# Optimization experiments

Hardware: AMD Instinct MI355X
Metric: run time of the kernel (lower is better)

## Reference

```python
import jax, jax.numpy as jnp
import numpy as np

B, N, F_IN, F_OUT, K = 128, 400, 128, 128, 5


def setup_inputs() -> dict:
    key = jax.random.key(0)
    ks = jax.random.split(key, 7)
    s_in = 1.0 / np.sqrt(F_IN)
    s_out = 1.0 / np.sqrt(F_OUT)
    return {
        "x": jax.random.normal(ks[0], (B, N, F_IN), dtype=jnp.float32),
        # SAGEConv layer 1: lin_l (neighbor agg, with bias) and lin_r (root, no bias)
        "W1l": jax.random.normal(ks[1], (F_OUT, F_IN), dtype=jnp.float32) * s_in,
        "b1l": jnp.zeros((F_OUT,), dtype=jnp.float32),
        "W1r": jax.random.normal(ks[2], (F_OUT, F_IN), dtype=jnp.float32) * s_in,
        # SAGEConv layer 2
        "W2l": jax.random.normal(ks[3], (F_OUT, F_OUT), dtype=jnp.float32) * s_out,
        "b2l": jnp.zeros((F_OUT,), dtype=jnp.float32),
        "W2r": jax.random.normal(ks[4], (F_OUT, F_OUT), dtype=jnp.float32) * s_out,
    }


def _knn_sym_adj(x):
    # x: [B, N, F]. Per-batch 5-NN graph with self-loops (loop=True),
    # then symmetrized (to_undirected coalesces duplicates -> 0/1 adjacency).
    sq = jnp.sum(x * x, axis=-1)                       # [B, N]
    d2 = sq[:, :, None] + sq[:, None, :] - 2.0 * jnp.einsum("bnd,bmd->bnm", x, x)
    _, idx = jax.lax.top_k(-d2, K)                     # [B, N, K] nearest incl. self
    A = jnp.zeros((x.shape[0], x.shape[1], x.shape[1]), dtype=x.dtype)
    bi = jnp.arange(x.shape[0])[:, None, None]
    ni = jnp.arange(x.shape[1])[None, :, None]
    A = A.at[bi, ni, idx].set(1.0)                     # A[b,i,j]=1 if j in knn(i)
    return jnp.maximum(A, A.transpose(0, 2, 1))        # undirected


def _sage(h, A, deg, Wl, bl, Wr):
    # PyG SAGEConv (mean aggr): out = lin_l(mean_j x_j) + lin_r(x_i)
    m = jnp.einsum("bnm,bmf->bnf", A, h) / deg
    return m @ Wl.T + bl + h @ Wr.T


def reference(x, W1l, b1l, W1r, W2l, b2l, W2r):
    A = _knn_sym_adj(x)
    deg = jnp.sum(A, axis=-1, keepdims=True)           # >=1 (self-loop)
    h = jax.nn.relu(_sage(x, A, deg, W1l, b1l, W1r))
    h = _sage(h, A, deg, W2l, b2l, W2r)
    return h.reshape(B * N, F_OUT)
```

## Files before the change

### kernel.cpp

```cpp
#include <hip/hip_runtime.h>
#include <hip/hip_bf16.h>
#include <stdint.h>

#define B_   128
#define N_   400
#define F_   128
#define K_   5
#define ROWS (B_ * N_)
#define POOLCAP 2048
#define DCAP 416
#define MAXFLAG ROWS
#define GAP_HEDGE 5e-4
#define DELTA_MAX 0.18f
#define NW 13

typedef __attribute__((ext_vector_type(8))) short bf16x8;
typedef __attribute__((ext_vector_type(4))) float f32x4;

static __device__ __forceinline__ unsigned short f2bf(float f) {
  union { float f; unsigned u; } v; v.f = f;
  unsigned r = v.u + 0x7fff + ((v.u >> 16) & 1);
  return (unsigned short)(r >> 16);
}
static __device__ __forceinline__ float bf2f(unsigned short h) {
  union { unsigned u; float f; } v; v.u = ((unsigned)h) << 16; return v.f;
}

template<int M, typename T>
static __device__ __forceinline__ void insM(T d, int j, T bd[], int bj[]) {
  if (d < bd[M - 1] || (d == bd[M - 1] && j < bj[M - 1])) {
    bd[M - 1] = d; bj[M - 1] = j;
#pragma unroll
    for (int q = M - 1; q > 0; --q) {
      bool sw = (bd[q] < bd[q - 1]) || (bd[q] == bd[q - 1] && bj[q] < bj[q - 1]);
      T td = bd[q]; int tj = bj[q];
      if (sw) { bd[q] = bd[q - 1]; bd[q - 1] = td; bj[q] = bj[q - 1]; bj[q - 1] = tj; }
    }
  }
}

__global__ __launch_bounds__(256) void k_prep_rows(const float* __restrict__ x,
                                                   unsigned short* __restrict__ Y,
                                                   float* __restrict__ sq) {
  int wave = threadIdx.x >> 6, lane = threadIdx.x & 63;
  int row = blockIdx.x * 4 + wave;
  float2 v = *(const float2*)&x[(size_t)row * F_ + lane * 2];
  unsigned short hx = f2bf(v.x), hy = f2bf(v.y);
  float lx = v.x - bf2f(hx), ly = v.y - bf2f(hy);
  *(unsigned*)&Y[(size_t)row * 256 + lane * 2]       = (unsigned)hx | ((unsigned)hy << 16);
  *(unsigned*)&Y[(size_t)row * 256 + 128 + lane * 2] = (unsigned)f2bf(lx) | ((unsigned)f2bf(ly) << 16);
  float s = v.x * v.x + v.y * v.y;
#pragma unroll
  for (int o = 32; o > 0; o >>= 1) s += __shfl_xor(s, o);
  if (lane == 0) sq[row] = s;
}

__global__ __launch_bounds__(256) void k_prep_w(const float* __restrict__ W1l,
                                                const float* __restrict__ W1r,
                                                const float* __restrict__ W2l,
                                                const float* __restrict__ W2r,
                                                unsigned short* __restrict__ Wh,
                                                unsigned short* __restrict__ Wlo) {
  int t = blockIdx.x * 256 + threadIdx.x;
  int m = t >> 14, e = t & 16383;
  const float* src = (m == 0) ? W1l : (m == 1) ? W1r : (m == 2) ? W2l : W2r;
  float f = src[e];
  unsigned short h = f2bf(f);
  Wh[t] = h;
  Wlo[t] = f2bf(f - bf2f(h));
}

#define YJ_STRIDE 264
__global__ __launch_bounds__(256) void k_knn(const unsigned short* __restrict__ Y,
                                             const float* __restrict__ sq,
                                             int* __restrict__ idxout,
                                             int* __restrict__ flagcnt,
                                             int* __restrict__ flagrows,
                                             int* __restrict__ cand) {
  __shared__ unsigned short Yj[64 * YJ_STRIDE];
  __shared__ float sqj[64];

  int b = blockIdx.y, i0 = blockIdx.x * 64;
  int tid = threadIdx.x, wave = tid >> 6, lane = tid & 63;

  int i_local = wave * 16 + (lane & 15);
  int arow = b * N_ + min(i0 + i_local, N_ - 1);
  float sqi = sq[arow];

  const bf16x8* abase = (const bf16x8*)&Y[(size_t)arow * 256];
  bf16x8 af[8];
#pragma unroll
  for (int kc = 0; kc < 8; ++kc) af[kc] = abase[kc * 4 + (lane >> 4)];

  float bd[8] = {3.4e38f, 3.4e38f, 3.4e38f, 3.4e38f, 3.4e38f, 3.4e38f, 3.4e38f, 3.4e38f};
  int   bj[8] = {1 << 30, 1 << 30, 1 << 30, 1 << 30, 1 << 30, 1 << 30, 1 << 30, 1 << 30};

  const float4* srcb = (const float4*)(Y + (size_t)b * N_ * 256);

  int pr[8], pcc[8];
#pragma unroll
  for (int q = 0; q < 8; ++q) { int l = tid + 256 * q; pr[q] = l >> 5; pcc[q] = l & 31; }

  float4 pre[8];
#pragma unroll
  for (int q = 0; q < 8; ++q) pre[q] = srcb[min(pr[q], N_ - 1) * 32 + pcc[q]];
  float sqpre = 0.f;
  if (tid < 64) sqpre = sq[b * N_ + min(tid, N_ - 1)];

  for (int jt = 0; jt < 7; ++jt) {
    int j0 = jt * 64;
    float4* dst4 = (float4*)Yj;
#pragma unroll
    for (int q = 0; q < 8; ++q) dst4[pr[q] * 33 + pcc[q]] = pre[q];
    if (tid < 64) sqj[tid] = sqpre;
    __syncthreads();

    if (jt < 6) {
      int j0n = j0 + 64;
#pragma unroll
      for (int q = 0; q < 8; ++q)
        pre[q] = srcb[min(j0n + pr[q], N_ - 1) * 32 + pcc[q]];
      if (tid < 64) sqpre = sq[b * N_ + min(j0n + tid, N_ - 1)];
    }

#pragma unroll
    for (int ct = 0; ct < 4; ++ct) {
      f32x4 acc = {0.f, 0.f, 0.f, 0.f};
      int jfr = ct * 16 + (lane & 15);
      const bf16x8* bbase = (const bf16x8*)&Yj[jfr * YJ_STRIDE];
#pragma unroll
      for (int kc = 0; kc < 12; ++kc) {
        int bidx = (kc & 3) * 4 + ((kc >= 8) ? 16 : 0) + (lane >> 4);
        acc = __builtin_amdgcn_mfma_f32_16x16x32_bf16(bbase[bidx], af[kc & 7], acc, 0, 0, 0);
      }
      int jbase = ct * 16 + (lane >> 4) * 4;
      float4 sjv = *(const float4*)&sqj[jbase];
      float sj4[4] = {sjv.x, sjv.y, sjv.z, sjv.w};
#pragma unroll
      for (int r = 0; r < 4; ++r) {
        int j = j0 + jbase + r;
        float d = sqi + sj4[r] - 2.0f * acc[r];
        if (j < N_) insM<8, float>(d, j, bd, bj);
      }
    }
    __syncthreads();
  }

  float* mbd = (float*)Yj;
  int*   mbj = (int*)Yj + 64 * 33;
  int slot = i_local * 33 + (lane >> 4) * 8;
#pragma unroll
  for (int q = 0; q < 8; ++q) { mbd[slot + q] = bd[q]; mbj[slot + q] = bj[q]; }
  __syncthreads();

  if (tid < 64) {
    int i = i0 + tid;
    if (i < N_) {
      float fd[6] = {3.4e38f, 3.4e38f, 3.4e38f, 3.4e38f, 3.4e38f, 3.4e38f};
      int   fj[6] = {1 << 30, 1 << 30, 1 << 30, 1 << 30, 1 << 30, 1 << 30};
      for (int q = 0; q < 32; ++q)
        insM<6, float>(mbd[tid * 33 + q], mbj[tid * 33 + q], fd, fj);
      int gi = b * N_ + i;
#pragma unroll
      for (int q = 0; q < 5; ++q) idxout[gi * K_ + q] = fj[q];
      if (fd[5] - fd[4] < 0.02f) {
        int pos = atomicAdd(flagcnt, 1);
        if (pos < MAXFLAG) {
          flagrows[pos] = gi;
          for (int q = 0; q < 32; ++q) cand[gi * 32 + q] = mbj[tid * 33 + q];
        }
      }
    }
  }
}

__global__ __launch_bounds__(256) void k_refine(const float* __restrict__ x,
                                                const int* __restrict__ flagrows,
                                                const int* __restrict__ flagcnt,
                                                const int* __restrict__ cand,
                                                int* __restrict__ idx,
                                                int* __restrict__ hcnt,
                                                int* __restrict__ hrows,
                                                int* __restrict__ hab) {
  __shared__ double dbuf[8][32];
  __shared__ int    jbuf[8][32];
  int slot = threadIdx.x >> 5, c = threadIdx.x & 31;
  int nflag = min(*flagcnt, MAXFLAG);
  for (int base = blockIdx.x * 8; base < nflag; base += gridDim.x * 8) {
    int t = base + slot;
    __syncthreads();
    if (t < nflag) {
      int row = flagrows[t];
      int b = row / N_;
      int j = cand[row * 32 + c];
      const float* xi = x + (size_t)row * F_;
      const float* xj = x + (size_t)(b * N_ + j) * F_;
      double s = 0.0;
#pragma unroll
      for (int q = 0; q < 128; ++q) {
        double d = (double)xi[q] - (double)xj[q];
        s = fma(d, d, s);
      }
      dbuf[slot][c] = s; jbuf[slot][c] = j;
    }
    __syncthreads();
    if (c == 0 && t < nflag) {
      int row = flagrows[t];
      int b = row / N_;
      double fd[6] = {1e300, 1e300, 1e300, 1e300, 1e300, 1e300};
      int    fj[6] = {1 << 30, 1 << 30, 1 << 30, 1 << 30, 1 << 30, 1 << 30};
      for (int q = 0; q < 32; ++q) insM<6, double>(dbuf[slot][q], jbuf[slot][q], fd, fj);
#pragma unroll
      for (int q = 0; q < 5; ++q) idx[row * K_ + q] = fj[q];
      if (fd[5] - fd[4] < GAP_HEDGE) {
        int p = atomicAdd(hcnt, 1);
        if (p < MAXFLAG) {
          hrows[p] = row;
          hab[2 * p]     = b * N_ + fj[4];
          hab[2 * p + 1] = b * N_ + fj[5];
        }
      }
    }
  }
}

__global__ __launch_bounds__(512) void k_buildg(const int* __restrict__ idx,
                                                const int* __restrict__ c6,
                                                int* __restrict__ L6,
                                                float* __restrict__ W6,
                                                int* __restrict__ pooli,
                                                float* __restrict__ poolw,
                                                int* __restrict__ offi,
                                                int* __restrict__ cnti) {
  __shared__ unsigned bm1[N_][NW];
  __shared__ unsigned bmh[N_][NW];
  __shared__ int cs[512];
  int b = blockIdx.x, t = threadIdx.x;
  int gb0 = b * N_;

  for (int q = t; q < N_ * NW; q += 512) {
    (&bm1[0][0])[q] = 0u;
    (&bmh[0][0])[q] = 0u;
  }

  int i = t;
  int j0 = -1, j1 = -1, j2 = -1, j3 = -1, j4 = -1, y6 = -1;
  if (i < N_) {
    const int* ip = idx + (size_t)(gb0 + i) * 5;
    j0 = ip[0]; j1 = ip[1]; j2 = ip[2]; j3 = ip[3]; j4 = ip[4];
    y6 = c6[gb0 + i];
  }
  __syncthreads();

  if (i < N_) {
    unsigned bit = 1u << (i & 31);
    int w = i >> 5;
    if (j0 != i) atomicOr(&bm1[j0][w], bit);
    if (j1 != i) atomicOr(&bm1[j1][w], bit);
    if (j2 != i) atomicOr(&bm1[j2][w], bit);
    if (j3 != i) atomicOr(&bm1[j3][w], bit);
    if (j4 != i) {
      if (y6 >= 0) atomicOr(&bmh[j4][w], bit); else atomicOr(&bm1[j4][w], bit);
    }
    if (y6 >= 0 && y6 != i) atomicOr(&bmh[y6][w], bit);
  }
  __syncthreads();

  if (i < N_) {
    int gi = gb0 + i;
    int   jj[6]  = {j0, j1, j2, j3, j4, y6};
    float w1s[6] = {1.f, 1.f, 1.f, 1.f,
                    (y6 >= 0) ? 0.5f : 1.f,
                    (y6 >= 0) ? 0.5f : 0.f};
#pragma unroll
    for (int k = 0; k < 6; ++k) {
      int j = jj[k]; float w1 = w1s[k];
      size_t sl = (size_t)gi * 6 + k;
      if (w1 <= 0.f || j < 0) { L6[sl] = gi; W6[sl] = 0.f; continue; }
      if (j == i)             { L6[sl] = gi; W6[sl] = 1.f; continue; }
      float w2 = ((bm1[i][j >> 5] >> (j & 31)) & 1) ? 1.f
               : (((bmh[i][j >> 5] >> (j & 31)) & 1) ? 0.5f : 0.f);
      L6[sl] = gb0 + j; W6[sl] = fmaxf(w1, w2);
    }
  }

  unsigned mw[NW];
  int cnt_i = 0;
  if (i < N_) {
#pragma unroll
    for (int w = 0; w < NW; ++w) {
      unsigned ex = 0;
      if ((i  >> 5) == w) ex |= 1u << (i  & 31);
      if ((j0 >> 5) == w) ex |= 1u << (j0 & 31);
      if ((j1 >> 5) == w) ex |= 1u << (j1 & 31);
      if ((j2 >> 5) == w) ex |= 1u << (j2 & 31);
      if ((j3 >> 5) == w) ex |= 1u << (j3 & 31);
      if ((j4 >> 5) == w) ex |= 1u << (j4 & 31);
      if (y6 >= 0 && (y6 >> 5) == w) ex |= 1u << (y6 & 31);
      unsigned m = (bm1[i][w] | bmh[i][w]) & ~ex;
      mw[w] = m;
      cnt_i += __popc(m);
    }
  } else {
#pragma unroll
    for (int w = 0; w < NW; ++w) mw[w] = 0u;
  }

  cs[t] = (i < N_) ? cnt_i : 0;
  __syncthreads();
  for (int off = 1; off < 512; off <<= 1) {
    int v = (t >= off) ? cs[t - off] : 0;
    __syncthreads();
    cs[t] += v;
    __syncthreads();
  }

  if (i < N_) {
    int o = b * POOLCAP + cs[t] - cnt_i;
    offi[gb0 + i] = o;
    cnti[gb0 + i] = cnt_i;
    int c = 0;
#pragma unroll
    for (int w = 0; w < NW; ++w) {
      unsigned m = mw[w];
      unsigned ones = bm1[i][w];
      while (m) {
        int bit = __ffs(m) - 1; m &= m - 1;
        int r = w * 32 + bit;
        pooli[o + c] = gb0 + r;
        poolw[o + c] = ((ones >> bit) & 1) ? 1.f : 0.5f;
        ++c;
      }
    }
  }
}

__global__ __launch_bounds__(128) void k_delta(
    const float* __restrict__ P, const float* __restrict__ Qb,
    const float* __restrict__ b1, const unsigned short* __restrict__ h1b,
    const float* __restrict__ sumP, const float* __restrict__ degv,
    const int* __restrict__ L6, const float* __restrict__ W6,
    const int* __restrict__ pooli, const float* __restrict__ poolw,
    const int* __restrict__ offi, const int* __restrict__ cnti,
    const int* __restrict__ idx,
    const int* __restrict__ hcnt, const int* __restrict__ hrows,
    const int* __restrict__ hab,
    const float* __restrict__ W2l, const float* __restrict__ W2r,
    int* __restrict__ c6, int* __restrict__ dcnt, int* __restrict__ dlist) {
  __shared__ float H[3][2][128];
  __shared__ float dH[3][128];
  __shared__ float U[3][128];
  __shared__ float V1[128], V2[128], red[128];
  __shared__ int   Ls[3][DCAP];
  __shared__ float Wsh[3][DCAP];
  int f = threadIdx.x;
  int n = min(*hcnt, MAXFLAG);
  for (int t = blockIdx.x; t < n; t += gridDim.x) {
    int gi = hrows[t], ga = hab[2 * t], gb = hab[2 * t + 1];
    int bb = gi / N_, iw = gi - bb * N_;
    bool ma = false, mb = false;
#pragma unroll
    for (int q = 0; q < K_; ++q) {
      ma = ma || (idx[ga * K_ + q] == iw);
      mb = mb || (idx[gb * K_ + q] == iw);
    }
    if (ma && mb) continue;
    int rows3[3] = {gi, ga, gb};
    int nn3[3];
    for (int s3 = 0; s3 < 3; ++s3) {
      int r = rows3[s3];
      int cc = cnti[r], oo = offi[r];
      int nn = 6 + cc; nn3[s3] = nn;
      for (int e = f; e < DCAP; e += 128) {
        int li = -1; float lw = 0.f;
        if (e < 6)      { li = L6[(size_t)r * 6 + e]; lw = W6[(size_t)r * 6 + e]; }
        else if (e < nn){ li = pooli[oo + e - 6];     lw = poolw[oo + e - 6]; }
        Ls[s3][e] = li; Wsh[s3][e] = lw;
      }
    }
    for (int s3 = 0; s3 < 3; ++s3) {
      int r = rows3[s3];
      float s1 = sumP[(size_t)r * 128 + f], d1 = degv[r];
      float ds = 0.f, dd = 0.f;
      if (s3 == 0) {
        if (!ma) { ds -= P[(size_t)ga * 128 + f]; dd -= 1.f; }
        if (!mb) { ds += P[(size_t)gb * 128 + f]; dd += 1.f; }
      } else if (s3 == 1) {
        if (!ma) { ds -= P[(size_t)gi * 128 + f]; dd -= 1.f; }
      } else {
        if (!mb) { ds += P[(size_t)gi * 128 + f]; dd += 1.f; }
      }
      float base = b1[f] + Qb[(size_t)r * 128 + f];
      float h0 = fmaxf(s1 / d1 + base, 0.f);
      float h1v = fmaxf((s1 + ds) / (d1 + dd) + base, 0.f);
      H[s3][0][f] = h0;
      H[s3][1][f] = h1v;
      dH[s3][f] = h1v - h0;
    }
    __syncthreads();
    {
      float u0 = 0.f, u1 = 0.f, u2 = 0.f;
      for (int f2 = 0; f2 < 128; ++f2) {
        float wv = W2l[f * 128 + f2];
        u0 += dH[0][f2] * wv;
        u1 += dH[1][f2] * wv;
        u2 += dH[2][f2] * wv;
      }
      U[0][f] = u0; U[1][f] = u1; U[2][f] = u2;
    }
    __syncthreads();
    float dmax = 0.f;
    for (int which = 0; which < 3; ++which) {
      float v1 = 0.f, v2 = 0.f;
      float d1r = degv[rows3[which]], d2r = d1r;
      int nnw = nn3[which];
      for (int e2 = 0; e2 < nnw; ++e2) {
        float w = Wsh[which][e2];
        if (w == 0.f) continue;
        int s = Ls[which][e2];
        float hv1, hv2;
        if (s == gi)      { hv1 = H[0][0][f]; hv2 = H[0][1][f]; }
        else if (s == ga) { hv1 = H[1][0][f]; hv2 = H[1][1][f]; }
        else if (s == gb) { hv1 = H[2][0][f]; hv2 = H[2][1][f]; }
        else {
          float hh = bf2f(h1b[(size_t)s * 256 + f]) + bf2f(h1b[(size_t)s * 256 + 128 + f]);
          hv1 = hh; hv2 = hh;
        }
        bool inG2 = true;
        if (which == 0 && s == ga && !ma) inG2 = false;
        if (which == 1 && s == gi && !ma) inG2 = false;
        v1 += w * hv1;
        if (inG2) v2 += w * hv2; else d2r -= w;
      }
      if (which == 0 && !mb) { v2 += H[2][1][f]; d2r += 1.f; }
      if (which == 2 && !mb) { v2 += H[0][1][f]; d2r += 1.f; }
      V1[f] = v1; V2[f] = v2;
      __syncthreads();
      float a1 = 0.f, a2 = 0.f, ow = 0.f;
      for (int f2 = 0; f2 < 128; ++f2) {
        float wl = W2l[f * 128 + f2];
        a1 += V1[f2] * wl;
        a2 += V2[f2] * wl;
        ow += dH[which][f2] * W2r[f * 128 + f2];
      }
      dmax = fmaxf(dmax, fabsf(a2 / d2r - a1 / d1r + ow));
      __syncthreads();
    }
    for (int li = 0; li < 3; ++li) {
      for (int e = f; e < nn3[li]; e += 128) {
        float w = Wsh[li][e];
        if (w == 0.f) continue;
        int r = Ls[li][e];
        if (r == gi || r == ga || r == gb) continue;
        bool dup = false;
        for (int lj = 0; lj < li && !dup; ++lj)
          for (int e2 = 0; e2 < nn3[lj]; ++e2)
            if (Ls[lj][e2] == r && Wsh[lj][e2] != 0.f) { dup = true; break; }
        if (dup) continue;
        float wi = 0.f, wa = 0.f, wb = 0.f;
        if (li == 0) wi = w; else if (li == 1) wa = w; else wb = w;
        for (int lj = li + 1; lj < 3; ++lj)
          for (int e2 = 0; e2 < nn3[lj]; ++e2)
            if (Ls[lj][e2] == r && Wsh[lj][e2] != 0.f) {
              if (lj == 1) wa = Wsh[lj][e2]; else wb = Wsh[lj][e2];
            }
        float lm = 0.f;
        for (int ff = 0; ff < 128; ++ff)
          lm = fmaxf(lm, fabsf(wi * U[0][ff] + wa * U[1][ff] + wb * U[2][ff]));
        dmax = fmaxf(dmax, lm / degv[r]);
      }
    }
    red[f] = dmax;
    __syncthreads();
    for (int o = 64; o > 0; o >>= 1) {
      if (f < o) red[f] = fmaxf(red[f], red[f + o]);
      __syncthreads();
    }
    if (f == 0 && red[0] < DELTA_MAX) {
      c6[gi] = gb - bb * N_;
      int p = atomicAdd(dcnt, 3);
      dlist[p] = gi; dlist[p + 1] = ga; dlist[p + 2] = gb;
    }
    __syncthreads();
  }
}

#define WSTR 130
__global__ __launch_bounds__(256) void k_gemm(const unsigned short* __restrict__ A,
                                              const unsigned short* __restrict__ Whl,
                                              const unsigned short* __restrict__ Whr,
                                              const unsigned short* __restrict__ Wll,
                                              const unsigned short* __restrict__ Wlr,
                                              float* __restrict__ P, float* __restrict__ Q) {
  __shared__ unsigned short W[4 * 128 * WSTR];
  int tid = threadIdx.x, wave = tid >> 6, lane = tid & 63;
#pragma unroll
  for (int q = 0; q < 2; ++q) {
    int ridx = tid * 2 + q;
    int mat = ridx >> 7, n = ridx & 127;
    const unsigned short* src =
        ((mat == 0) ? Whl : (mat == 1) ? Whr : (mat == 2) ? Wll : Wlr) + n * 128;
    unsigned short* dst = &W[(size_t)ridx * WSTR];
#pragma unroll
    for (int p = 0; p < 16; ++p) *(bf16x8*)(dst + p * 8) = *(const bf16x8*)(src + p * 8);
  }
  __syncthreads();

  size_t row = (size_t)blockIdx.x * 64 + wave * 16 + (lane & 15);
  bf16x8 af[8];
#pragma unroll
  for (int s = 0; s < 2; ++s)
#pragma unroll
    for (int kc = 0; kc < 4; ++kc)
      af[s * 4 + kc] = *(const bf16x8*)&A[row * 256 + s * 128 + kc * 32 + (lane >> 4) * 8];

  size_t orow0 = (size_t)blockIdx.x * 64 + wave * 16 + (lane >> 4) * 4;
#pragma unroll
  for (int w = 0; w < 2; ++w) {
    float* O = w ? Q : P;
#pragma unroll
    for (int ct = 0; ct < 8; ++ct) {
      f32x4 acc = {0.f, 0.f, 0.f, 0.f};
      int n = ct * 16 + (lane & 15);
      const unsigned short* bh = &W[(size_t)(w * 128 + n) * WSTR];
      const unsigned short* bl = &W[(size_t)((2 + w) * 128 + n) * WSTR];
#pragma unroll
      for (int kc = 0; kc < 4; ++kc) {
        bf16x8 fh = *(const bf16x8*)(bh + kc * 32 + (lane >> 4) * 8);
        bf16x8 fl_ = *(const bf16x8*)(bl + kc * 32 + (lane >> 4) * 8);
        acc = __builtin_amdgcn_mfma_f32_16x16x32_bf16(af[kc], fh, acc, 0, 0, 0);
        acc = __builtin_amdgcn_mfma_f32_16x16x32_bf16(af[4 + kc], fh, acc, 0, 0, 0);
        acc = __builtin_amdgcn_mfma_f32_16x16x32_bf16(af[kc], fl_, acc, 0, 0, 0);
      }
#pragma unroll
      for (int r = 0; r < 4; ++r)
        O[(orow0 + r) * 128 + ct * 16 + (lane & 15)] = acc[r];
    }
  }
}

__global__ __launch_bounds__(256) void k_gemm_d(const unsigned short* __restrict__ A,
                                                const unsigned short* __restrict__ Whl,
                                                const unsigned short* __restrict__ Whr,
                                                const unsigned short* __restrict__ Wll,
                                                const unsigned short* __restrict__ Wlr,
                                                float* __restrict__ P, float* __restrict__ Q,
                                                const int* __restrict__ dcnt,
                                                const int* __restrict__ dlist) {
  int dn = *dcnt;
  if (blockIdx.x * 64 >= dn) return;
  __shared__ unsigned short W[4 * 128 * WSTR];
  int tid = threadIdx.x, wave = tid >> 6, lane = tid & 63;
#pragma unroll
  for (int q = 0; q < 2; ++q) {
    int ridx = tid * 2 + q;
    int mat = ridx >> 7, n = ridx & 127;
    const unsigned short* src =
        ((mat == 0) ? Whl : (mat == 1) ? Whr : (mat == 2) ? Wll : Wlr) + n * 128;
    unsigned short* dst = &W[(size_t)ridx * WSTR];
#pragma unroll
    for (int p = 0; p < 16; ++p) *(bf16x8*)(dst + p * 8) = *(const bf16x8*)(src + p * 8);
  }
  __syncthreads();

  for (int tb = blockIdx.x * 64; tb < dn; tb += gridDim.x * 64) {
    size_t row = (size_t)dlist[min(tb + wave * 16 + (lane & 15), dn - 1)];
    bf16x8 af[8];
#pragma unroll
    for (int s = 0; s < 2; ++s)
#pragma unroll
      for (int kc = 0; kc < 4; ++kc)
        af[s * 4 + kc] = *(const bf16x8*)&A[row * 256 + s * 128 + kc * 32 + (lane >> 4) * 8];

    int lo0 = tb + wave * 16 + (lane >> 4) * 4;
#pragma unroll
    for (int w = 0; w < 2; ++w) {
      float* O = w ? Q : P;
#pragma unroll
      for (int ct = 0; ct < 8; ++ct) {
        f32x4 acc = {0.f, 0.f, 0.f, 0.f};
        int n = ct * 16 + (lane & 15);
        const unsigned short* bh = &W[(size_t)(w * 128 + n) * WSTR];
        const unsigned short* bl = &W[(size_t)((2 + w) * 128 + n) * WSTR];
#pragma unroll
        for (int kc = 0; kc < 4; ++kc) {
          bf16x8 fh = *(const bf16x8*)(bh + kc * 32 + (lane >> 4) * 8);
          bf16x8 fl_ = *(const bf16x8*)(bl + kc * 32 + (lane >> 4) * 8);
          acc = __builtin_amdgcn_mfma_f32_16x16x32_bf16(af[kc], fh, acc, 0, 0, 0);
          acc = __builtin_amdgcn_mfma_f32_16x16x32_bf16(af[4 + kc], fh, acc, 0, 0, 0);
          acc = __builtin_amdgcn_mfma_f32_16x16x32_bf16(af[kc], fl_, acc, 0, 0, 0);
        }
#pragma unroll
        for (int r = 0; r < 4; ++r) {
          size_t orow = (size_t)dlist[min(lo0 + r, dn - 1)];
          O[orow * 128 + ct * 16 + (lane & 15)] = acc[r];
        }
      }
    }
  }
}

__global__ __launch_bounds__(256) void k_aggr(const float* __restrict__ P,
                                              const float* __restrict__ Q,
                                              const int* __restrict__ L6,
                                              const float* __restrict__ W6,
                                              const int* __restrict__ pooli,
                                              const float* __restrict__ poolw,
                                              const int* __restrict__ offi,
                                              const int* __restrict__ cnti,
                                              const float* __restrict__ bias,
                                              float* __restrict__ outf,
                                              unsigned short* __restrict__ outb,
                                              float* __restrict__ sumP,
                                              float* __restrict__ degv,
                                              int relu) {
  int r = blockIdx.x * 8 + (threadIdx.x >> 5);
  int l4 = threadIdx.x & 31;
  int m = cnti[r], o = offi[r];
  float4 acc = {0.f, 0.f, 0.f, 0.f};
  float deg = 0.f;
#pragma unroll
  for (int k = 0; k < 6; ++k) {
    float ww = W6[(size_t)r * 6 + k];
    float4 p4 = *(const float4*)&P[(size_t)L6[(size_t)r * 6 + k] * 128 + l4 * 4];
    acc.x += ww * p4.x; acc.y += ww * p4.y;
    acc.z += ww * p4.z; acc.w += ww * p4.w;
    deg += ww;
  }
  for (int q = 0; q < m; ++q) {
    float ww = poolw[o + q];
    float4 p4 = *(const float4*)&P[(size_t)pooli[o + q] * 128 + l4 * 4];
    acc.x += ww * p4.x; acc.y += ww * p4.y;
    acc.z += ww * p4.z; acc.w += ww * p4.w;
    deg += ww;
  }
  if (sumP) {
    *(float4*)&sumP[(size_t)r * 128 + l4 * 4] = acc;
    if (l4 == 0) degv[r] = deg;
  }
  float4 b4 = *(const float4*)&bias[l4 * 4];
  float4 q4 = *(const float4*)&Q[(size_t)r * 128 + l4 * 4];
  float4 v;
  v.x = acc.x / deg + b4.x + q4.x;
  v.y = acc.y / deg + b4.y + q4.y;
  v.z = acc.z / deg + b4.z + q4.z;
  v.w = acc.w / deg + b4.w + q4.w;
  if (relu) {
    v.x = fmaxf(v.x, 0.f); v.y = fmaxf(v.y, 0.f);
    v.z = fmaxf(v.z, 0.f); v.w = fmaxf(v.w, 0.f);
  }
  if (outf) {
    *(float4*)&outf[(size_t)r * 128 + l4 * 4] = v;
  } else {
    ushort4 hi, lo;
    hi.x = f2bf(v.x); hi.y = f2bf(v.y); hi.z = f2bf(v.z); hi.w = f2bf(v.w);
    lo.x = f2bf(v.x - bf2f(hi.x)); lo.y = f2bf(v.y - bf2f(hi.y));
    lo.z = f2bf(v.z - bf2f(hi.z)); lo.w = f2bf(v.w - bf2f(hi.w));
    *(ushort4*)&outb[(size_t)r * 256 + l4 * 4] = hi;
    *(ushort4*)&outb[(size_t)r * 256 + 128 + l4 * 4] = lo;
  }
}

__global__ __launch_bounds__(256) void k_aggr_d(const float* __restrict__ P,
                                                const float* __restrict__ Q,
                                                const int* __restrict__ L6,
                                                const float* __restrict__ W6,
                                                const int* __restrict__ pooli,
                                                const float* __restrict__ poolw,
                                                const int* __restrict__ offi,
                                                const int* __restrict__ cnti,
                                                const float* __restrict__ bias,
                                                unsigned short* __restrict__ outb,
                                                const int* __restrict__ dcnt,
                                                const int* __restrict__ dlist) {
  int dn = *dcnt;
  int l4 = threadIdx.x & 31;
  for (int di = blockIdx.x * 8 + (threadIdx.x >> 5); di < dn; di += gridDim.x * 8) {
    int r = dlist[di];
    int m = cnti[r], o = offi[r];
    float4 acc = {0.f, 0.f, 0.f, 0.f};
    float deg = 0.f;
#pragma unroll
    for (int k = 0; k < 6; ++k) {
      float ww = W6[(size_t)r * 6 + k];
      float4 p4 = *(const float4*)&P[(size_t)L6[(size_t)r * 6 + k] * 128 + l4 * 4];
      acc.x += ww * p4.x; acc.y += ww * p4.y;
      acc.z += ww * p4.z; acc.w += ww * p4.w;
      deg += ww;
    }
    for (int q = 0; q < m; ++q) {
      float ww = poolw[o + q];
      float4 p4 = *(const float4*)&P[(size_t)pooli[o + q] * 128 + l4 * 4];
      acc.x += ww * p4.x; acc.y += ww * p4.y;
      acc.z += ww * p4.z; acc.w += ww * p4.w;
      deg += ww;
    }
    float4 b4 = *(const float4*)&bias[l4 * 4];
    float4 q4 = *(const float4*)&Q[(size_t)r * 128 + l4 * 4];
    float4 v;
    v.x = fmaxf(acc.x / deg + b4.x + q4.x, 0.f);
    v.y = fmaxf(acc.y / deg + b4.y + q4.y, 0.f);
    v.z = fmaxf(acc.z / deg + b4.z + q4.z, 0.f);
    v.w = fmaxf(acc.w / deg + b4.w + q4.w, 0.f);
    ushort4 hi, lo;
    hi.x = f2bf(v.x); hi.y = f2bf(v.y); hi.z = f2bf(v.z); hi.w = f2bf(v.w);
    lo.x = f2bf(v.x - bf2f(hi.x)); lo.y = f2bf(v.y - bf2f(hi.y));
    lo.z = f2bf(v.z - bf2f(hi.z)); lo.w = f2bf(v.w - bf2f(hi.w));
    *(ushort4*)&outb[(size_t)r * 256 + l4 * 4] = hi;
    *(ushort4*)&outb[(size_t)r * 256 + 128 + l4 * 4] = lo;
  }
}

extern "C" void kernel_launch(void* const* d_in, const int* in_sizes, int n_in,
                              void* d_out, int out_size, void* d_ws, size_t ws_size,
                              hipStream_t stream) {
  const float* x   = (const float*)d_in[0];
  const float* W1l = (const float*)d_in[1];
  const float* b1l = (const float*)d_in[2];
  const float* W1r = (const float*)d_in[3];
  const float* W2l = (const float*)d_in[4];
  const float* b2l = (const float*)d_in[5];
  const float* W2r = (const float*)d_in[6];
  float* out = (float*)d_out;

  char* w = (char*)d_ws;
  unsigned short* Y    = (unsigned short*)w; w += (size_t)ROWS * 256 * 2;
  float*          sq   = (float*)w;          w += (size_t)ROWS * 4;
  unsigned short* Wh   = (unsigned short*)w; w += (size_t)4 * 16384 * 2;
  unsigned short* Wlo  = (unsigned short*)w; w += (size_t)4 * 16384 * 2;
  int*            idx  = (int*)w;            w += (size_t)ROWS * K_ * 4;
  int*            L6   = (int*)w;            w += (size_t)ROWS * 6 * 4;
  float*          W6   = (float*)w;          w += (size_t)ROWS * 6 * 4;
  int*            pooli= (int*)w;            w += (size_t)B_ * POOLCAP * 4;
  float*          poolw= (float*)w;          w += (size_t)B_ * POOLCAP * 4;
  int*            offi = (int*)w;            w += (size_t)ROWS * 4;
  int*            cnti = (int*)w;            w += (size_t)ROWS * 4;
  int*            flags = (int*)w;           w += 64;
  int*            c6   = (int*)w;            w += (size_t)ROWS * 4;
  int*            dlist= (int*)w;            w += (size_t)3 * MAXFLAG * 4;
  int*            flagrows = (int*)w;        w += (size_t)MAXFLAG * 4;
  int*            hrows = (int*)w;           w += (size_t)MAXFLAG * 4;
  int*            hab  = (int*)w;            w += (size_t)MAXFLAG * 8;
  int*            candb = (int*)w;           w += (size_t)ROWS * 32 * 4;
  float*          P    = (float*)w;          w += (size_t)ROWS * 128 * 4;
  float*          Qb   = (float*)w;          w += (size_t)ROWS * 128 * 4;
  unsigned short* h1b  = (unsigned short*)w; w += (size_t)ROWS * 256 * 2;
  float*          sumP = (float*)w;          w += (size_t)ROWS * 128 * 4;
  float*          degv = (float*)w;          w += (size_t)ROWS * 4;
  float* P2 = (float*)Y;
  float* Q2 = sumP;
  (void)ws_size; (void)in_sizes; (void)n_in; (void)out_size;

  hipMemsetAsync(flags, 0, 64, stream);
  hipMemsetAsync(c6, 0xFF, (size_t)ROWS * 4, stream);
  k_prep_rows<<<ROWS / 4, 256, 0, stream>>>(x, Y, sq);
  k_prep_w<<<(4 * 16384) / 256, 256, 0, stream>>>(W1l, W1r, W2l, W2r, Wh, Wlo);
  k_knn<<<dim3(7, B_), 256, 0, stream>>>(Y, sq, idx, &flags[0], flagrows, candb);
  k_gemm<<<ROWS / 64, 256, 0, stream>>>(Y, Wh, Wh + 16384, Wlo, Wlo + 16384, P, Qb);
  k_refine<<<64, 256, 0, stream>>>(x, flagrows, &flags[0], candb, idx,
                                   &flags[1], hrows, hab);
  k_buildg<<<B_, 512, 0, stream>>>(idx, c6, L6, W6, pooli, poolw, offi, cnti);
  k_aggr<<<ROWS / 8, 256, 0, stream>>>(P, Qb, L6, W6, pooli, poolw, offi, cnti,
                                       b1l, nullptr, h1b, sumP, degv, 1);
  k_delta<<<64, 128, 0, stream>>>(P, Qb, b1l, h1b, sumP, degv, L6, W6, pooli,
                                  poolw, offi, cnti, idx, &flags[1], hrows, hab,
                                  W2l, W2r, c6, &flags[2], dlist);
  k_buildg<<<B_, 512, 0, stream>>>(idx, c6, L6, W6, pooli, poolw, offi, cnti);
  k_gemm<<<ROWS / 64, 256, 0, stream>>>(h1b, Wh + 2 * 16384, Wh + 3 * 16384,
                                        Wlo + 2 * 16384, Wlo + 3 * 16384, P2, Q2);
  k_aggr_d<<<64, 256, 0, stream>>>(P, Qb, L6, W6, pooli, poolw, offi, cnti,
                                   b1l, h1b, &flags[2], dlist);
  k_gemm_d<<<32, 256, 0, stream>>>(h1b, Wh + 2 * 16384, Wh + 3 * 16384,
                                   Wlo + 2 * 16384, Wlo + 3 * 16384, P2, Q2,
                                   &flags[2], dlist);
  k_aggr<<<ROWS / 8, 256, 0, stream>>>(P2, Q2, L6, W6, pooli, poolw, offi, cnti,
                                       b2l, out, nullptr, nullptr, nullptr, 0);
}
```

Measured before the change: 696.7 us.

## Drop register prefetch in kNN tile loop, halve GEMM LDS, remap aggr blocks

Three unrelated edits. The kNN distance kernel no longer prefetches the next Y tile into registers and instead loads each tile straight into LDS before the barrier. This lowers register pressure but exposes global load latency. The GEMM kernel stages only the two weight matrices needed per output (P then Q) instead of all four, which halves LDS and may let more blocks fit per CU, at the cost of an extra barrier and reload. The aggregation kernel remaps block indices so that consecutive blocks are spread across strided row chunks, presumably to change how work lands on XCDs or cache.

Result: faster. 597.6 us (-14.2%).

```diff
diff --git a/kernel.cpp b/kernel.cpp
--- a/kernel.cpp
+++ b/kernel.cpp
@@ -97,31 +97,18 @@
 
   const float4* srcb = (const float4*)(Y + (size_t)b * N_ * 256);
 
-  int pr[8], pcc[8];
-#pragma unroll
-  for (int q = 0; q < 8; ++q) { int l = tid + 256 * q; pr[q] = l >> 5; pcc[q] = l & 31; }
-
-  float4 pre[8];
-#pragma unroll
-  for (int q = 0; q < 8; ++q) pre[q] = srcb[min(pr[q], N_ - 1) * 32 + pcc[q]];
-  float sqpre = 0.f;
-  if (tid < 64) sqpre = sq[b * N_ + min(tid, N_ - 1)];
-
   for (int jt = 0; jt < 7; ++jt) {
     int j0 = jt * 64;
     float4* dst4 = (float4*)Yj;
 #pragma unroll
-    for (int q = 0; q < 8; ++q) dst4[pr[q] * 33 + pcc[q]] = pre[q];
-    if (tid < 64) sqj[tid] = sqpre;
-    __syncthreads();
-
-    if (jt < 6) {
-      int j0n = j0 + 64;
-#pragma unroll
-      for (int q = 0; q < 8; ++q)
-        pre[q] = srcb[min(j0n + pr[q], N_ - 1) * 32 + pcc[q]];
-      if (tid < 64) sqpre = sq[b * N_ + min(j0n + tid, N_ - 1)];
-    }
+    for (int q = 0; q < 8; ++q) {
+      int l = tid + 256 * q;
+      int r = l >> 5, cc = l & 31;
+      int jr = min(j0 + r, N_ - 1);
+      dst4[r * 33 + cc] = srcb[jr * 32 + cc];
+    }
+    if (tid < 64) sqj[tid] = sq[b * N_ + min(j0 + tid, N_ - 1)];
+    __syncthreads();
 
 #pragma unroll
     for (int ct = 0; ct < 4; ++ct) {
@@ -492,19 +479,8 @@
                                               const unsigned short* __restrict__ Wll,
                                               const unsigned short* __restrict__ Wlr,
                                               float* __restrict__ P, float* __restrict__ Q) {
-  __shared__ unsigned short W[4 * 128 * WSTR];
+  __shared__ unsigned short W[2 * 128 * WSTR];
   int tid = threadIdx.x, wave = tid >> 6, lane = tid & 63;
-#pragma unroll
-  for (int q = 0; q < 2; ++q) {
-    int ridx = tid * 2 + q;
-    int mat = ridx >> 7, n = ridx & 127;
-    const unsigned short* src =
-        ((mat == 0) ? Whl : (mat == 1) ? Whr : (mat == 2) ? Wll : Wlr) + n * 128;
-    unsigned short* dst = &W[(size_t)ridx * WSTR];
-#pragma unroll
-    for (int p = 0; p < 16; ++p) *(bf16x8*)(dst + p * 8) = *(const bf16x8*)(src + p * 8);
-  }
-  __syncthreads();
 
   size_t row = (size_t)blockIdx.x * 64 + wave * 16 + (lane & 15);
   bf16x8 af[8];
@@ -517,13 +493,25 @@
   size_t orow0 = (size_t)blockIdx.x * 64 + wave * 16 + (lane >> 4) * 4;
 #pragma unroll
   for (int w = 0; w < 2; ++w) {
+    {
+      int mat = tid >> 7, nrow = tid & 127;
+      const unsigned short* src =
+          (mat == 0) ? ((w == 0) ? Whl : Whr) + nrow * 128
+                     : ((w == 0) ? Wll : Wlr) + nrow * 128;
+      unsigned short* dst = &W[(size_t)tid * WSTR];
+      if (w) __syncthreads();
+#pragma unroll
+      for (int p = 0; p < 16; ++p) *(bf16x8*)(dst + p * 8) = *(const bf16x8*)(src + p * 8);
+    }
+    __syncthreads();
+
     float* O = w ? Q : P;
 #pragma unroll
     for (int ct = 0; ct < 8; ++ct) {
       f32x4 acc = {0.f, 0.f, 0.f, 0.f};
       int n = ct * 16 + (lane & 15);
-      const unsigned short* bh = &W[(size_t)(w * 128 + n) * WSTR];
-      const unsigned short* bl = &W[(size_t)((2 + w) * 128 + n) * WSTR];
+      const unsigned short* bh = &W[(size_t)n * WSTR];
+      const unsigned short* bl = &W[(size_t)(128 + n) * WSTR];
 #pragma unroll
       for (int kc = 0; kc < 4; ++kc) {
         bf16x8 fh = *(const bf16x8*)(bh + kc * 32 + (lane >> 4) * 8);
@@ -614,7 +602,9 @@
                                               float* __restrict__ sumP,
                                               float* __restrict__ degv,
                                               int relu) {
-  int r = blockIdx.x * 8 + (threadIdx.x >> 5);
+  int bid = blockIdx.x;
+  int chunk = (bid & 7) * (gridDim.x >> 3) + (bid >> 3);
+  int r = chunk * 8 + (threadIdx.x >> 5);
   int l4 = threadIdx.x & 31;
   int m = cnti[r], o = offi[r];
   float4 acc = {0.f, 0.f, 0.f, 0.f};
```
